# Optimization experiments

Measured on AMD Instinct MI355X. Metric: run time of the kernel, lower is better.

The kernel has to match this reference:

```python
import jax, jax.numpy as jnp
import numpy as np

V, E, H, C, T = 100000, 300, 512, 40, 4096  # vocab, embed, hidden, num_classes, seq_len


def setup_inputs() -> dict:
    key = jax.random.key(0)
    ks = jax.random.split(key, 19)
    s = lambda k, shape: jax.random.normal(k, shape, jnp.float32) * 0.05
    inp = {"x": jax.random.randint(ks[0], (T,), 0, V, dtype=jnp.int32)}
    inp["emb"] = s(ks[1], (V, E))  # frozen embedding table
    # PyTorch LSTM params, gate order (i, f, g, o); layer0 in=E, layer1 in=2H
    inp["Wih0f"] = s(ks[2], (4 * H, E)); inp["Whh0f"] = s(ks[3], (4 * H, H)); inp["b0f"] = s(ks[4], (4 * H,))
    inp["Wih0b"] = s(ks[5], (4 * H, E)); inp["Whh0b"] = s(ks[6], (4 * H, H)); inp["b0b"] = s(ks[7], (4 * H,))
    inp["Wih1f"] = s(ks[8], (4 * H, 2 * H)); inp["Whh1f"] = s(ks[9], (4 * H, H)); inp["b1f"] = s(ks[10], (4 * H,))
    inp["Wih1b"] = s(ks[11], (4 * H, 2 * H)); inp["Whh1b"] = s(ks[12], (4 * H, H)); inp["b1b"] = s(ks[13], (4 * H,))
    inp["Wc"] = s(ks[14], (C, 2 * H)); inp["bc"] = s(ks[15], (C,))
    inp["trans"] = s(ks[16], (C, C))  # CRF transitions prev->next
    inp["start"] = s(ks[17], (C,)); inp["end"] = s(ks[18], (C,))
    return inp


def _lstm_dir(x, Wih, Whh, b, reverse):
    # x: (T, D) unbatched; returns hidden states (T, H)
    Hd = Whh.shape[1]
    def step(carry, xt):
        h, c = carry
        g = xt @ Wih.T + h @ Whh.T + b  # (4H,)
        i, f, gg, o = jnp.split(g, 4)
        i = jax.nn.sigmoid(i); f = jax.nn.sigmoid(f)
        gg = jnp.tanh(gg); o = jax.nn.sigmoid(o)
        c = f * c + i * gg
        h = o * jnp.tanh(c)
        return (h, c), h
    xs = x[::-1] if reverse else x
    init = (jnp.zeros((Hd,), x.dtype), jnp.zeros((Hd,), x.dtype))
    _, hs = jax.lax.scan(step, init, xs)
    return hs[::-1] if reverse else hs


def _viterbi(emissions, trans, start, end):
    # emissions: (T, C); returns best path (T,) int32
    def fwd(score, em):
        m = score[:, None] + trans  # (C_prev, C_next)
        bp = jnp.argmax(m, axis=0).astype(jnp.int32)
        return jnp.max(m, axis=0) + em, bp
    score0 = start + emissions[0]
    final, bps = jax.lax.scan(fwd, score0, emissions[1:])  # bps: (T-1, C)
    last = jnp.argmax(final + end).astype(jnp.int32)
    def back(tag, bp):
        prev = bp[tag]
        return prev, prev
    _, path = jax.lax.scan(back, last, bps, reverse=True)  # tags 0..T-2 in order
    return jnp.concatenate([path, last[None]])


def reference(x, emb, Wih0f, Whh0f, b0f, Wih0b, Whh0b, b0b, Wih1f, Whh1f, b1f, Wih1b, Whh1b, b1b, Wc, bc, trans, start, end):
    e = emb[x]  # (T, E); dropout is identity at eval
    h0 = jnp.concatenate([_lstm_dir(e, Wih0f, Whh0f, b0f, False),
                          _lstm_dir(e, Wih0b, Whh0b, b0b, True)], axis=-1)  # (T, 2H)
    h1 = jnp.concatenate([_lstm_dir(h0, Wih1f, Whh1f, b1f, False),
                          _lstm_dir(h0, Wih1b, Whh1b, b1b, True)], axis=-1)  # (T, 2H)
    o = h1 @ Wc.T + bc  # (T, C)
    tag_scores = jax.nn.log_softmax(o, axis=1)
    tags = _viterbi(tag_scores, trans, start, end)
    return tag_scores, tags
```

## Files before the change

### kernel.cpp

```cpp
#include <hip/hip_runtime.h>


typedef unsigned int u32;
typedef unsigned long long u64;
typedef u32 u32x4 __attribute__((ext_vector_type(4)));
typedef __attribute__((ext_vector_type(8))) short s16x8;
typedef __attribute__((ext_vector_type(4))) float f32x4;

#define TT 4096
#define HH 512
#define CC 40
#define NG 2048

__device__ __forceinline__ float sigm(float x) { return 1.0f / (1.0f + __expf(-x)); }
__device__ __forceinline__ float tanh_(float x) { return 1.0f - 2.0f / (__expf(2.0f * x) + 1.0f); }

__device__ __forceinline__ void st_sys_u32(u32* p, u32 v) {
    asm volatile("global_store_dword %0, %1, off sc0 sc1"
                 :
                 : "v"(p), "v"(v)
                 : "memory");
}

__device__ __forceinline__ void ld_mall_b256(const float* p, u32x4& r0, u32x4& r1) {
    asm volatile(
        "global_load_dwordx4 %0, %2, off sc0 sc1\n\t"
        "global_load_dwordx4 %1, %2, off offset:16 sc0 sc1\n\t"
        "s_waitcnt vmcnt(0)"
        : "=&v"(r0), "=&v"(r1)
        : "v"(p)
        : "memory");
}

__device__ __forceinline__ void split_pack8(const float* f, s16x8& hi, s16x8& lo) {
#pragma unroll
    for (int j = 0; j < 8; j++) {
        float x = f[j];
        u32 h = __float_as_uint(x) & 0xFFFF0000u;
        float hf = __uint_as_float(h);
        hi[j] = (short)(h >> 16);
        lo[j] = (short)(__float_as_uint(x - hf) >> 16);
    }
}

__global__ __launch_bounds__(256, 2) void gemm_bf16s_k(const float* __restrict__ A0,
                                                       const float* __restrict__ A1,
                                                       const int* __restrict__ xidx,
                                                       const float* __restrict__ W,
                                                       const float* __restrict__ bias,
                                                       float* __restrict__ C,
                                                       int M, int N, int K, int Ksplit) {
    __shared__ __align__(16) short sAh[128 * 32];
    __shared__ __align__(16) short sAl[128 * 32];
    __shared__ __align__(16) short sWh[128 * 32];
    __shared__ __align__(16) short sWl[128 * 32];
    const int tid = threadIdx.x;
    const int bn = blockIdx.x, bm = blockIdx.y;
    const int wid = tid >> 6, lane = tid & 63;
    const int qm = (wid >> 1) * 64, qn = (wid & 1) * 64;
    const int fr = lane & 15, fq = lane >> 4;

    const int srow = tid >> 1;
    const int kh = (tid & 1) * 16;

    const int am = bm * 128 + srow;
    const float* arow = xidx ? (A0 + (size_t)xidx[am] * K) : nullptr;
    const float* a0r = xidx ? nullptr : (A0 + (size_t)am * Ksplit);
    const float* a1r = xidx ? nullptr : (A1 + (size_t)am * Ksplit);
    const float* wrow = W + (size_t)(bn * 128 + srow) * K;

    f32x4 acc[4][4] = {};

    const int NP = (K + 31) >> 5;
    for (int kp = 0; kp < NP; kp++) {
        const int kb = kp * 32 + kh;
        float fa[16], fw[16];
        if (kb + 16 <= K) {
#pragma unroll
            for (int j = 0; j < 16; j += 4) {
                int k = kb + j;
                const float* s = xidx ? (arow + k)
                                      : ((k < Ksplit) ? (a0r + k) : (a1r + (k - Ksplit)));
                float4 v = *(const float4*)s;
                fa[j] = v.x; fa[j + 1] = v.y; fa[j + 2] = v.z; fa[j + 3] = v.w;
                float4 wv = *(const float4*)(wrow + k);
                fw[j] = wv.x; fw[j + 1] = wv.y; fw[j + 2] = wv.z; fw[j + 3] = wv.w;
            }
        } else {
#pragma unroll
            for (int j = 0; j < 16; j++) {
                int k = kb + j;
                float av = 0.f, wv = 0.f;
                if (k < K) {
                    av = xidx ? arow[k] : ((k < Ksplit) ? a0r[k] : a1r[k - Ksplit]);
                    wv = wrow[k];
                }
                fa[j] = av; fw[j] = wv;
            }
        }
        __syncthreads();
#pragma unroll
        for (int c = 0; c < 2; c++) {
            int ch = (tid & 1) * 2 + c;
            int pch = ch ^ ((srow >> 1) & 3);
            int off = srow * 32 + pch * 8;
            s16x8 hi, lo;
            split_pack8(fa + c * 8, hi, lo);
            *(s16x8*)&sAh[off] = hi;
            *(s16x8*)&sAl[off] = lo;
            split_pack8(fw + c * 8, hi, lo);
            *(s16x8*)&sWh[off] = hi;
            *(s16x8*)&sWl[off] = lo;
        }
        __syncthreads();

        s16x8 ah[4], al[4];
#pragma unroll
        for (int m = 0; m < 4; m++) {
            int row = qm + m * 16 + fr;
            int off = row * 32 + ((fq ^ ((row >> 1) & 3)) * 8);
            ah[m] = *(const s16x8*)&sAh[off];
            al[m] = *(const s16x8*)&sAl[off];
        }
#pragma unroll
        for (int n = 0; n < 4; n++) {
            int row = qn + n * 16 + fr;
            int off = row * 32 + ((fq ^ ((row >> 1) & 3)) * 8);
            s16x8 bh = *(const s16x8*)&sWh[off];
            s16x8 bl = *(const s16x8*)&sWl[off];
#pragma unroll
            for (int m = 0; m < 4; m++) {
                acc[m][n] = __builtin_amdgcn_mfma_f32_16x16x32_bf16(ah[m], bh, acc[m][n], 0, 0, 0);
                acc[m][n] = __builtin_amdgcn_mfma_f32_16x16x32_bf16(ah[m], bl, acc[m][n], 0, 0, 0);
                acc[m][n] = __builtin_amdgcn_mfma_f32_16x16x32_bf16(al[m], bh, acc[m][n], 0, 0, 0);
            }
        }
    }

#pragma unroll
    for (int n = 0; n < 4; n++) {
        int gcol = bn * 128 + qn + n * 16 + fr;
        float b = bias[gcol];
#pragma unroll
        for (int m = 0; m < 4; m++) {
            int rbase = bm * 128 + qm + m * 16 + fq * 4;
#pragma unroll
            for (int r2 = 0; r2 < 4; r2++)
                C[(size_t)(rbase + r2) * N + gcol] = acc[m][n][r2] + b;
        }
    }
}

__global__ __attribute__((amdgpu_flat_work_group_size(512, 512), amdgpu_waves_per_eu(2, 2)))
void lstm_phase_k(const float* __restrict__ WxF,
                  const float* __restrict__ WxB,
                  const float* __restrict__ WhhF,
                  const float* __restrict__ WhhB,
                  float* __restrict__ histF,
                  float* __restrict__ histB,
                  int phase) {
    const int wg = blockIdx.x & 31;
    const int dir = blockIdx.x >> 5;
    const int tid = threadIdx.x;
    const float* Wx = dir ? WxB : WxF;
    const float* Whh = dir ? WhhB : WhhF;
    float* hist = dir ? histB : histF;
    const u32 ENC = phase ? 0x7F800000u : 0u;

    const int r = tid >> 3, seg = tid & 7;
    const int grow = (r >> 4) * 512 + wg * 16 + (r & 15);

    float w[64];
    {
        const float* wr = Whh + (size_t)grow * HH + seg * 64;
#pragma unroll
        for (int i = 0; i < 16; i++) {
            float4 v = *(const float4*)(wr + i * 4);
            w[i * 4 + 0] = v.x; w[i * 4 + 1] = v.y; w[i * 4 + 2] = v.z; w[i * 4 + 3] = v.w;
        }
    }

    const int j = (tid < 62) ? (tid + (tid >= wg * 2 ? 2 : 0)) : 0;

    __shared__ float lds_h[8 * 68];
    __shared__ float lds_g[64];
    float c_state = 0.f;
    int capped = 0;

    for (int s = 0; s < TT; ++s) {
        const int t = dir ? (TT - 1 - s) : s;
        float wxv = 0.f;
        if (seg == 0) wxv = Wx[(size_t)t * NG + grow];

        if (s > 0) {
            const int tprev = dir ? (t + 1) : (t - 1);
            if (tid < 62) {
                const float* p = hist + (size_t)tprev * HH + j * 8;
                u32x4 v0, v1;
                if (!capped) {
                    int it = 0;
                    for (;;) {
                        ld_mall_b256(p, v0, v1);
                        bool ok;
                        if (phase) {
                            ok = ((v0.x & 0x7F800000u) >= 0x40000000u) &&
                                 ((v0.y & 0x7F800000u) >= 0x40000000u) &&
                                 ((v0.z & 0x7F800000u) >= 0x40000000u) &&
                                 ((v0.w & 0x7F800000u) >= 0x40000000u) &&
                                 ((v1.x & 0x7F800000u) >= 0x40000000u) &&
                                 ((v1.y & 0x7F800000u) >= 0x40000000u) &&
                                 ((v1.z & 0x7F800000u) >= 0x40000000u) &&
                                 ((v1.w & 0x7F800000u) >= 0x40000000u);
                        } else {
                            ok = (v0.x != 0xAAAAAAAAu) && (v0.y != 0xAAAAAAAAu) &&
                                 (v0.z != 0xAAAAAAAAu) && (v0.w != 0xAAAAAAAAu) &&
                                 (v1.x != 0xAAAAAAAAu) && (v1.y != 0xAAAAAAAAu) &&
                                 (v1.z != 0xAAAAAAAAu) && (v1.w != 0xAAAAAAAAu);
                        }
                        if (ok) break;
                        if (++it > (1 << 18)) { capped = 1; break; }
                    }
                } else {
                    ld_mall_b256(p, v0, v1);
                }
                float* dst = &lds_h[(j >> 3) * 68 + ((j & 7) * 8)];
                float4 f0, f1;
                f0.x = __uint_as_float(v0.x ^ ENC); f0.y = __uint_as_float(v0.y ^ ENC);
                f0.z = __uint_as_float(v0.z ^ ENC); f0.w = __uint_as_float(v0.w ^ ENC);
                f1.x = __uint_as_float(v1.x ^ ENC); f1.y = __uint_as_float(v1.y ^ ENC);
                f1.z = __uint_as_float(v1.z ^ ENC); f1.w = __uint_as_float(v1.w ^ ENC);
                *(float4*)dst = f0;
                *(float4*)(dst + 4) = f1;
            }
            __syncthreads();
            float a0 = 0.f, a1 = 0.f, a2 = 0.f, a3 = 0.f;
            const float4* hv4 = (const float4*)&lds_h[seg * 68];
#pragma unroll
            for (int i = 0; i < 16; i++) {
                float4 hv = hv4[i];
                a0 += w[i * 4 + 0] * hv.x;
                a1 += w[i * 4 + 1] * hv.y;
                a2 += w[i * 4 + 2] * hv.z;
                a3 += w[i * 4 + 3] * hv.w;
            }
            float acc = (a0 + a1) + (a2 + a3);
            acc += __shfl_xor(acc, 1);
            acc += __shfl_xor(acc, 2);
            acc += __shfl_xor(acc, 4);
            if (seg == 0) lds_g[r] = acc + wxv;
        } else {
            if (seg == 0) lds_g[r] = wxv;
        }
        __syncthreads();

        if (tid < 16) {
            float gi = lds_g[tid], gf = lds_g[16 + tid], gg = lds_g[32 + tid], go = lds_g[48 + tid];
            float iv = sigm(gi), fv = sigm(gf), gv = tanh_(gg), ov = sigm(go);
            c_state = fv * c_state + iv * gv;
            float h = ov * tanh_(c_state);
            int hidx = wg * 16 + tid;
            lds_h[(hidx >> 6) * 68 + (hidx & 63)] = h;
            st_sys_u32((u32*)&hist[(size_t)t * HH + hidx], __float_as_uint(h) ^ ENC);
        }
    }
}

__global__ __launch_bounds__(64, 4) void classifier_k(const float* __restrict__ histF,
                                                      const float* __restrict__ histB,
                                                      const float* __restrict__ Wc,
                                                      const float* __restrict__ bc,
                                                      float* __restrict__ outsc) {
    int t = blockIdx.x, lane = threadIdx.x;
    __shared__ float hrow[1024];
    const uint4* hf4 = (const uint4*)(histF + (size_t)t * HH);
    const uint4* hb4 = (const uint4*)(histB + (size_t)t * HH);
#pragma unroll
    for (int jj = 0; jj < 4; jj++) {
        int idx4 = jj * 64 + lane;
        uint4 u = (idx4 < 128) ? hf4[idx4] : hb4[idx4 - 128];
        u.x ^= 0x7F800000u; u.y ^= 0x7F800000u; u.z ^= 0x7F800000u; u.w ^= 0x7F800000u;
        float4 v;
        v.x = __uint_as_float(u.x); v.y = __uint_as_float(u.y);
        v.z = __uint_as_float(u.z); v.w = __uint_as_float(u.w);
        *(float4*)&hrow[idx4 * 4] = v;
    }
    __syncthreads();
    float o = 0.f;
    if (lane < CC) {
        o = bc[lane];
        const float4* wr = (const float4*)(Wc + (size_t)lane * 1024);
#pragma unroll 4
        for (int kk = 0; kk < 256; ++kk) {
            float4 w4 = wr[kk];
            float4 h4 = *(const float4*)&hrow[kk * 4];
            o += w4.x * h4.x + w4.y * h4.y + w4.z * h4.z + w4.w * h4.w;
        }
    }
    float m = (lane < CC) ? o : -1e30f;
#pragma unroll
    for (int d = 1; d < 64; d <<= 1) m = fmaxf(m, __shfl_xor(m, d));
    float ex = (lane < CC) ? __expf(o - m) : 0.f;
#pragma unroll
    for (int d = 1; d < 64; d <<= 1) ex += __shfl_xor(ex, d);
    float lse = m + __logf(ex);
    if (lane < CC) outsc[(size_t)t * CC + lane] = o - lse;
}

__global__ __launch_bounds__(64) void viterbi_k(const float* __restrict__ em,
                                               const float* __restrict__ trans,
                                               const float* __restrict__ startv,
                                               const float* __restrict__ endv,
                                               unsigned char* __restrict__ bp,
                                               float* __restrict__ outtags) {
    int lane = threadIdx.x;
    float tcol[CC];
#pragma unroll
    for (int p = 0; p < CC; p++) tcol[p] = 0.f;
    if (lane < CC) {
#pragma unroll
        for (int p = 0; p < CC; p++) tcol[p] = trans[p * CC + lane];
    }
    float s = (lane < CC) ? (startv[lane] + em[lane]) : 0.f;

    for (int t = 1; t < TT; ++t) {
        float emv = (lane < CC) ? em[(size_t)t * CC + lane] : 0.f;
        float b0 = -1e30f, b1 = -1e30f;
        int i0 = 0, i1 = 20;
#pragma unroll
        for (int p = 0; p < 20; p++) {
            float c0 = __shfl(s, p) + tcol[p];
            float c1 = __shfl(s, p + 20) + tcol[p + 20];
            if (c0 > b0) { b0 = c0; i0 = p; }
            if (c1 > b1) { b1 = c1; i1 = p + 20; }
        }
        float best = b0; int bi = i0;
        if (b1 > b0) { best = b1; bi = i1; }
        s = best + emv;
        if (lane < CC) bp[(size_t)t * CC + lane] = (unsigned char)bi;
    }
    float fv = (lane < CC) ? (s + endv[lane]) : -1e30f;
    int fi = (lane < CC) ? lane : 63;
#pragma unroll
    for (int d = 1; d < 64; d <<= 1) {
        float ov = __shfl_xor(fv, d);
        int oi = __shfl_xor(fi, d);
        if (ov > fv || (ov == fv && oi < fi)) { fv = ov; fi = oi; }
    }
    __threadfence();
    if (lane == 0) {
        int cur = fi;
        outtags[TT - 1] = (float)cur;
        for (int t = TT - 2; t >= 0; --t) {
            cur = bp[(size_t)(t + 1) * CC + cur];
            outtags[t] = (float)cur;
        }
    }
}

extern "C" void kernel_launch(void* const* d_in, const int* in_sizes, int n_in,
                              void* d_out, int out_size, void* d_ws, size_t ws_size,
                              hipStream_t stream) {
    const int*   x     = (const int*)d_in[0];
    const float* emb   = (const float*)d_in[1];
    const float* Wih0f = (const float*)d_in[2];
    const float* Whh0f = (const float*)d_in[3];
    const float* b0f   = (const float*)d_in[4];
    const float* Wih0b = (const float*)d_in[5];
    const float* Whh0b = (const float*)d_in[6];
    const float* b0b   = (const float*)d_in[7];
    const float* Wih1f = (const float*)d_in[8];
    const float* Whh1f = (const float*)d_in[9];
    const float* b1f   = (const float*)d_in[10];
    const float* Wih1b = (const float*)d_in[11];
    const float* Whh1b = (const float*)d_in[12];
    const float* b1b   = (const float*)d_in[13];
    const float* Wc    = (const float*)d_in[14];
    const float* bc    = (const float*)d_in[15];
    const float* trans = (const float*)d_in[16];
    const float* startv= (const float*)d_in[17];
    const float* endv  = (const float*)d_in[18];

    char* ws = (char*)d_ws;
    unsigned char* bp = (unsigned char*)(ws + 1024);
    float* WxF  = (float*)(ws + 262144);
    float* WxB  = (float*)(ws + 33816576);
    float* histF= (float*)(ws + 67371008);
    float* histB= (float*)(ws + 75759616);

    if (ws_size < (size_t)84148224) return;

    float* out_sc   = (float*)d_out;
    float* out_tags = out_sc + (size_t)TT * CC;

    gemm_bf16s_k<<<dim3(16, 32), 256, 0, stream>>>(emb, nullptr, x, Wih0f, b0f, WxF, TT, NG, 300, 300);
    gemm_bf16s_k<<<dim3(16, 32), 256, 0, stream>>>(emb, nullptr, x, Wih0b, b0b, WxB, TT, NG, 300, 300);
    lstm_phase_k<<<64, 512, 0, stream>>>(WxF, WxB, Whh0f, Whh0b, histF, histB, 0);
    gemm_bf16s_k<<<dim3(16, 32), 256, 0, stream>>>(histF, histB, nullptr, Wih1f, b1f, WxF, TT, NG, 1024, 512);
    gemm_bf16s_k<<<dim3(16, 32), 256, 0, stream>>>(histF, histB, nullptr, Wih1b, b1b, WxB, TT, NG, 1024, 512);
    lstm_phase_k<<<64, 512, 0, stream>>>(WxF, WxB, Whh1f, Whh1b, histF, histB, 1);
    classifier_k<<<TT, 64, 0, stream>>>(histF, histB, Wc, bc, out_sc);
    viterbi_k<<<1, 64, 0, stream>>>(out_sc, trans, startv, endv, bp, out_tags);
}
```

Before: 17.29 ms.

## Merge fwd/bwd input-projection GEMMs into one launch and prefetch next K tile

The forward and backward input-projection GEMMs now share one launch per layer, with blockIdx.z choosing the weight, bias and output pointers. This halves the GEMM launch count and doubles the blocks available for concurrency. The main loop also register-prefetches the next K tile's global loads after the shared-memory stores, so load latency overlaps the MFMA work. The extra live float arrays raise register pressure under the 2-blocks-per-CU launch bound.

Result: no change. 17.25 ms (-0.2%).

```diff
diff --git a/kernel.cpp b/kernel.cpp
--- a/kernel.cpp
+++ b/kernel.cpp
@@ -46,9 +46,12 @@
 __global__ __launch_bounds__(256, 2) void gemm_bf16s_k(const float* __restrict__ A0,
                                                        const float* __restrict__ A1,
                                                        const int* __restrict__ xidx,
-                                                       const float* __restrict__ W,
-                                                       const float* __restrict__ bias,
-                                                       float* __restrict__ C,
+                                                       const float* __restrict__ W0,
+                                                       const float* __restrict__ bias0,
+                                                       float* __restrict__ C0,
+                                                       const float* __restrict__ W1,
+                                                       const float* __restrict__ bias1,
+                                                       float* __restrict__ C1,
                                                        int M, int N, int K, int Ksplit) {
     __shared__ __align__(16) short sAh[128 * 32];
     __shared__ __align__(16) short sAl[128 * 32];
@@ -56,6 +59,9 @@
     __shared__ __align__(16) short sWl[128 * 32];
     const int tid = threadIdx.x;
     const int bn = blockIdx.x, bm = blockIdx.y;
+    const float* W    = blockIdx.z ? W1 : W0;
+    const float* bias = blockIdx.z ? bias1 : bias0;
+    float*       C    = blockIdx.z ? C1 : C0;
     const int wid = tid >> 6, lane = tid & 63;
     const int qm = (wid >> 1) * 64, qn = (wid & 1) * 64;
     const int fr = lane & 15, fq = lane >> 4;
@@ -71,10 +77,8 @@
 
     f32x4 acc[4][4] = {};
 
-    const int NP = (K + 31) >> 5;
-    for (int kp = 0; kp < NP; kp++) {
+    auto LOADP = [&](int kp, float* fa, float* fw) {
         const int kb = kp * 32 + kh;
-        float fa[16], fw[16];
         if (kb + 16 <= K) {
 #pragma unroll
             for (int j = 0; j < 16; j += 4) {
@@ -98,21 +102,33 @@
                 fa[j] = av; fw[j] = wv;
             }
         }
+    };
+
+    float fa[16], fw[16];
+    LOADP(0, fa, fw);
+
+    const int NP = (K + 31) >> 5;
+    for (int kp = 0; kp < NP; kp++) {
+        s16x8 hA[2], lA[2], hW[2], lW[2];
+#pragma unroll
+        for (int c = 0; c < 2; c++) {
+            split_pack8(fa + c * 8, hA[c], lA[c]);
+            split_pack8(fw + c * 8, hW[c], lW[c]);
+        }
         __syncthreads();
 #pragma unroll
         for (int c = 0; c < 2; c++) {
             int ch = (tid & 1) * 2 + c;
             int pch = ch ^ ((srow >> 1) & 3);
             int off = srow * 32 + pch * 8;
-            s16x8 hi, lo;
-            split_pack8(fa + c * 8, hi, lo);
-            *(s16x8*)&sAh[off] = hi;
-            *(s16x8*)&sAl[off] = lo;
-            split_pack8(fw + c * 8, hi, lo);
-            *(s16x8*)&sWh[off] = hi;
-            *(s16x8*)&sWl[off] = lo;
+            *(s16x8*)&sAh[off] = hA[c];
+            *(s16x8*)&sAl[off] = lA[c];
+            *(s16x8*)&sWh[off] = hW[c];
+            *(s16x8*)&sWl[off] = lW[c];
         }
         __syncthreads();
+
+        if (kp + 1 < NP) LOADP(kp + 1, fa, fw);
 
         s16x8 ah[4], al[4];
 #pragma unroll
@@ -392,11 +408,13 @@
     float* out_sc   = (float*)d_out;
     float* out_tags = out_sc + (size_t)TT * CC;
 
-    gemm_bf16s_k<<<dim3(16, 32), 256, 0, stream>>>(emb, nullptr, x, Wih0f, b0f, WxF, TT, NG, 300, 300);
-    gemm_bf16s_k<<<dim3(16, 32), 256, 0, stream>>>(emb, nullptr, x, Wih0b, b0b, WxB, TT, NG, 300, 300);
+    gemm_bf16s_k<<<dim3(16, 32, 2), 256, 0, stream>>>(emb, nullptr, x,
+                                                      Wih0f, b0f, WxF, Wih0b, b0b, WxB,
+                                                      TT, NG, 300, 300);
     lstm_phase_k<<<64, 512, 0, stream>>>(WxF, WxB, Whh0f, Whh0b, histF, histB, 0);
-    gemm_bf16s_k<<<dim3(16, 32), 256, 0, stream>>>(histF, histB, nullptr, Wih1f, b1f, WxF, TT, NG, 1024, 512);
-    gemm_bf16s_k<<<dim3(16, 32), 256, 0, stream>>>(histF, histB, nullptr, Wih1b, b1b, WxB, TT, NG, 1024, 512);
+    gemm_bf16s_k<<<dim3(16, 32, 2), 256, 0, stream>>>(histF, histB, nullptr,
+                                                      Wih1f, b1f, WxF, Wih1b, b1b, WxB,
+                                                      TT, NG, 1024, 512);
     lstm_phase_k<<<64, 512, 0, stream>>>(WxF, WxB, Whh1f, Whh1b, histF, histB, 1);
     classifier_k<<<TT, 64, 0, stream>>>(histF, histB, Wc, bc, out_sc);
     viterbi_k<<<1, 64, 0, stream>>>(out_sc, trans, startv, endv, bp, out_tags);
```
